# Kernel tuning notes

Measured on AMD Instinct MI355X. Metric: run time of the kernel, lower is better.

Reference implementation:

```python
import jax, jax.numpy as jnp
import numpy as np

N, E = 10000, 160000          # nodes, support edges
CIN, COUT = 32, 32            # channels
R, B = 6, 1                   # radial rings, band limit
M = 2 * B + 1                 # angular frequencies (-B..B)
EPS = 1e-8
PI = float(np.pi)


def _cplx(a):
    # (..., 2) real -> complex64
    return jax.lax.complex(a[..., 0], a[..., 1])


def _reim(z):
    # complex -> (..., 2) real
    return jnp.stack([jnp.real(z), jnp.imag(z)], axis=-1)


def _field_conv(xc, edges, stenc, w, off):
    """FieldConv (ftype=1): real radial/angular weights with per-channel phase offsets.
    xc: (N,Cin) complex, stenc: (E,R,M) complex stencil (transport+quadrature pre-multiplied),
    w: (R,M,Cin,Cout) real, off: (Cin,Cout) phase offsets."""
    Wc = w * jax.lax.complex(jnp.cos(off), jnp.sin(off))[None, None]   # (R,M,Cin,Cout) complex
    src, tgt = edges[:, 0], edges[:, 1]
    # edge gather + complex stencil multiply: (E,R,M,Cin)
    contrib = stenc[:, :, :, None] * xc[src][:, None, None, :]
    # scatter-add to target nodes: (N,R,M,Cin)
    agg = jax.ops.segment_sum(contrib, tgt, num_segments=N)
    # dense per-node filter contraction
    return jnp.einsum('nrmc,rmcd->nd', agg, Wc)


def _tangent_nonlin(xc, b):
    # magnitude ReLU with learned bias, direction preserved (complex tangent features)
    mag = jnp.abs(xc)
    return (jax.nn.relu(mag + b) / jnp.maximum(mag, EPS)) * xc


def _forward(x, supp_edges, supp_sten, w1, off1, b1, w2, off2, b2, res_w):
    xc = _cplx(x)                # (N,CIN) complex64
    stenc = _cplx(supp_sten)     # (E,R,M) complex64
    h = _tangent_nonlin(_field_conv(xc, supp_edges, stenc, w1, off1), b1)
    h = _field_conv(h, supp_edges, stenc, w2, off2)
    y = _tangent_nonlin(xc @ _cplx(res_w) + h, b2)   # residual TangentLin + nonlin
    return _reim(y)              # (N,COUT,2) float32


def setup_inputs() -> dict:
    key = jax.random.key(0)
    ks = jax.random.split(key, 10)
    s1 = 1.0 / np.sqrt(R * M * CIN)
    s2 = 1.0 / np.sqrt(R * M * COUT)
    return {
        'x': jax.random.normal(ks[0], (N, CIN, 2), jnp.float32),
        'supp_edges': jax.random.randint(ks[1], (E, 2), 0, N),
        'supp_sten': 0.1 * jax.random.normal(ks[2], (E, R, M, 2), jnp.float32),
        'w1': s1 * jax.random.normal(ks[3], (R, M, CIN, COUT), jnp.float32),
        'off1': jax.random.uniform(ks[4], (CIN, COUT), jnp.float32, -PI, PI),
        'b1': 0.1 * jax.random.normal(ks[5], (COUT,), jnp.float32),
        'w2': s2 * jax.random.normal(ks[6], (R, M, COUT, COUT), jnp.float32),
        'off2': jax.random.uniform(ks[7], (COUT, COUT), jnp.float32, -PI, PI),
        'b2': 0.1 * jax.random.normal(ks[8], (COUT,), jnp.float32),
        'res_w': (1.0 / np.sqrt(CIN)) * jax.random.normal(ks[9], (CIN, COUT, 2), jnp.float32),
    }


def reference(x, supp_edges, supp_sten, w1, off1, b1, w2, off2, b2, res_w):
    return _forward(x, supp_edges, supp_sten, w1, off1, b1, w2, off2, b2, res_w)
```

## Files before the change

### kernel.cpp

```cpp
#include <hip/hip_runtime.h>
#include <hip/hip_bf16.h>

#define NN   10000
#define EE   160000
#define CINC 32
#define COUTC 32
#define RRR  6
#define MMM  3
#define RM   (RRR*MMM)
#define KK   (RM*CINC)
#define KE   608
#define NPB  4
#define CAP  64
#define AROW 624
#define WSZ  19456
#define EPSV 1e-8f

typedef __attribute__((ext_vector_type(8))) short bf16x8;
typedef __attribute__((ext_vector_type(4))) float f32x4;
typedef __attribute__((ext_vector_type(16))) float f32x16;

__device__ inline short f2bf(float f) {
    __hip_bfloat16 b = __float2bfloat16(f);
    union { __hip_bfloat16 b; short s; } u; u.b = b;
    return u.s;
}
__device__ inline float bf2f(unsigned short h) {
    return __uint_as_float(((unsigned)h) << 16);
}
__device__ inline uint2 packsplit(float re, float im) {
    unsigned short rh = (unsigned short)f2bf(re);
    unsigned short rl = (unsigned short)f2bf(re - bf2f(rh));
    unsigned short ih = (unsigned short)f2bf(im);
    unsigned short il = (unsigned short)f2bf(im - bf2f(ih));
    return make_uint2((unsigned)rh | ((unsigned)rl << 16),
                      (unsigned)ih | ((unsigned)il << 16));
}

__global__ void __launch_bounds__(256)
k_build(const int* __restrict__ edges, int* __restrict__ cursor,
        const float* __restrict__ w1, const float* __restrict__ off1,
        const float* __restrict__ w2, const float* __restrict__ off2,
        short* __restrict__ Wcb1, short* __restrict__ Wcb2,
        int2* __restrict__ sei,
        const float2* __restrict__ xc, uint2* __restrict__ xbf,
        const float2* __restrict__ resw)
{
    int i = blockIdx.x*blockDim.x + threadIdx.x;
    if (i < KK*COUTC) {
        int d = i & 31;
        int k = i >> 5;
        int c = k & 31;
        int r_ = k >> 5;
        int q  = (k >> 3) & 3;
        int kk = k & 7;
        int l  = q*16 + (d & 15);
        int n2 = d >> 4;
        int addr = ((r_*2 + n2)*64 + l)*8 + kk;
        float o1 = off1[c*COUTC + d];
        float o2 = off2[c*COUTC + d];
        float s1 = sinf(o1), c1 = cosf(o1);
        float s2 = sinf(o2), c2 = cosf(o2);
        Wcb1[addr]       = f2bf(w1[i]*c1);
        Wcb1[WSZ + addr] = f2bf(w1[i]*s1);
        Wcb2[addr]       = f2bf(w2[i]*c2);
        Wcb2[WSZ + addr] = f2bf(w2[i]*s2);
    }
    if (i < 1024) {
        int n2 = i >> 9;
        int l2 = (i >> 3) & 63;
        int kk = i & 7;
        int c  = ((l2 >> 4) << 3) + kk;
        int d  = (n2 << 4) + (l2 & 15);
        int addr = ((18*2 + n2)*64 + l2)*8 + kk;
        float2 rv = resw[c*COUTC + d];
        Wcb2[addr]       = f2bf(rv.x);
        Wcb2[WSZ + addr] = f2bf(rv.y);
        Wcb1[addr]       = 0;
        Wcb1[WSZ + addr] = 0;
    }
    if (i < EE) {
        int src = edges[2*i];
        int tgt = edges[2*i+1];
        int pos = atomicAdd(&cursor[tgt], 1);
        if (pos < CAP) sei[tgt*CAP + pos] = make_int2(src, i);
    }
    if (i < NN*CINC) {
        float2 v = xc[i];
        xbf[i] = packsplit(v.x, v.y);
    }
}

template<bool FINAL>
__global__ void __launch_bounds__(256, 4)
k_conv(const uint2* __restrict__ xbf,
       const int*  __restrict__ cnts,
       const int2* __restrict__ sei,
       const float4* __restrict__ stenc4,
       const short* __restrict__ Wcb,
       const float* __restrict__ bias,
       const float2* __restrict__ xres,
       float2* __restrict__ out,
       uint2* __restrict__ outbf)
{
    __shared__ __align__(16) short aggS[2*NPB*AROW];
    int t = threadIdx.x;
    int g = t >> 6;
    int l = t & 63;
    int c = l & 31;
    int oct = l >> 5;
    int n = blockIdx.x*NPB + g;

    f32x16 Pre = (f32x16)(0.f), Pim = (f32x16)(0.f);
    {
        int2 v0 = make_int2(0, 0);
        if (l < 32) v0 = sei[n*CAP + l];
        int cnt = cnts[n]; if (cnt > CAP) cnt = CAP;
        if (l >= 32 && l < cnt) v0 = sei[n*CAP + l];
        int srcAll = (l < cnt) ? v0.x : 0;
        int eidAll = (l < cnt) ? v0.y : 0;

        bool rmok = (c < RM);
        int rmo = ((c >> 1) << 4) + ((c & 1) << 3);
        const char* sb = (const char*)stenc4;
        int ntiles = (cnt + 15) >> 4;

        union P { unsigned u[4]; short s[8]; bf16x8 v; };
        float2 sv[8], svn[8];
        uint2  xv[8], xvn[8];

        auto tload = [&](int ck, float2* svp, uint2* xvp) {
            int ebase = ck*16 + oct*8;
            #pragma unroll
            for (int j = 0; j < 8; ++j) {
                int e = ebase + j;
                int eid = __shfl(eidAll, e, 64);
                int s   = __shfl(srcAll, e, 64);
                bool ok = rmok && (e < cnt);
                float2 vv = make_float2(0.f, 0.f);
                if (ok) vv = *(const float2*)(sb + (size_t)eid*144 + rmo);
                svp[j] = vv;
                xvp[j] = xbf[(s << 5) | c];
            }
        };
        auto tcompute = [&](const float2* svp, const uint2* xvp) {
            P Are, Aim, AimN;
            #pragma unroll
            for (int j = 0; j < 8; ++j) {
                Are.s[j] = f2bf(svp[j].x);
                Aim.s[j] = f2bf(svp[j].y);
            }
            #pragma unroll
            for (int k2 = 0; k2 < 4; ++k2) AimN.u[k2] = Aim.u[k2] ^ 0x80008000u;
            P B;
            #pragma unroll
            for (int k2 = 0; k2 < 4; ++k2)
                B.u[k2] = (xvp[2*k2].x & 0xffffu) | (xvp[2*k2+1].x << 16);
            Pre = __builtin_amdgcn_mfma_f32_32x32x16_bf16(Are.v, B.v, Pre, 0, 0, 0);
            Pim = __builtin_amdgcn_mfma_f32_32x32x16_bf16(Aim.v, B.v, Pim, 0, 0, 0);
            #pragma unroll
            for (int k2 = 0; k2 < 4; ++k2)
                B.u[k2] = (xvp[2*k2].x >> 16) | (xvp[2*k2+1].x & 0xffff0000u);
            Pre = __builtin_amdgcn_mfma_f32_32x32x16_bf16(Are.v, B.v, Pre, 0, 0, 0);
            Pim = __builtin_amdgcn_mfma_f32_32x32x16_bf16(Aim.v, B.v, Pim, 0, 0, 0);
            #pragma unroll
            for (int k2 = 0; k2 < 4; ++k2)
                B.u[k2] = (xvp[2*k2].y & 0xffffu) | (xvp[2*k2+1].y << 16);
            Pre = __builtin_amdgcn_mfma_f32_32x32x16_bf16(AimN.v, B.v, Pre, 0, 0, 0);
            Pim = __builtin_amdgcn_mfma_f32_32x32x16_bf16(Are.v, B.v, Pim, 0, 0, 0);
            #pragma unroll
            for (int k2 = 0; k2 < 4; ++k2)
                B.u[k2] = (xvp[2*k2].y >> 16) | (xvp[2*k2+1].y & 0xffff0000u);
            Pre = __builtin_amdgcn_mfma_f32_32x32x16_bf16(AimN.v, B.v, Pre, 0, 0, 0);
            Pim = __builtin_amdgcn_mfma_f32_32x32x16_bf16(Are.v, B.v, Pim, 0, 0, 0);
        };

        if (ntiles > 0) {
            tload(0, sv, xv);
            for (int ck = 0; ck < ntiles; ++ck) {
                bool more = (ck + 1 < ntiles);
                if (more) tload(ck+1, svn, xvn);
                tcompute(sv, xv);
                if (more) {
                    #pragma unroll
                    for (int j = 0; j < 8; ++j) { sv[j] = svn[j]; xv[j] = xvn[j]; }
                }
            }
        }

        short* aR = aggS + g*AROW;
        short* aI = aggS + NPB*AROW + g*AROW;
        #pragma unroll
        for (int reg = 0; reg < 16; ++reg) {
            int rm = (reg & 3) + 8*(reg >> 2) + 4*oct;
            if (rm < RM) {
                aR[rm*32 + c] = f2bf(Pre[reg]);
                aI[rm*32 + c] = f2bf(Pim[reg]);
            }
        }
        if (l < 32) {
            float2 xvv = make_float2(0.f, 0.f);
            if (FINAL) xvv = xres[(size_t)n*CINC + l];
            aR[KK + l] = f2bf(xvv.x);
            aI[KK + l] = f2bf(xvv.y);
        }
    }
    __syncthreads();

    int quad = l >> 4;
    int nn16 = l & 15;
    int mrow = (nn16 < NPB) ? nn16 : NPB-1;
    int rm0 = (g < 3) ? 5*g : 15;
    int nrm = (g < 3) ? 5 : 4;
    const short* aggR = aggS;
    const short* aggI = aggS + NPB*AROW;
    const short* Wr = Wcb;
    const short* Wi = Wcb + WSZ;
    int lbase = l*8;

    f32x4 Dre[2], Dim[2];
    #pragma unroll
    for (int nt = 0; nt < 2; ++nt) { Dre[nt] = (f32x4)(0.f); Dim[nt] = (f32x4)(0.f); }
    union PU { unsigned u[4]; bf16x8 v; };
    for (int r = rm0; r < rm0 + nrm; ++r) {
        int koff = r*32 + quad*8;
        bf16x8 ar = *(const bf16x8*)(aggR + mrow*AROW + koff);
        PU ai, ain;
        ai.v = *(const bf16x8*)(aggI + mrow*AROW + koff);
        #pragma unroll
        for (int k2 = 0; k2 < 4; ++k2) ain.u[k2] = ai.u[k2] ^ 0x80008000u;
        #pragma unroll
        for (int nt = 0; nt < 2; ++nt) {
            int woff = ((r*2 + nt) << 9) + lbase;
            bf16x8 br = *(const bf16x8*)(Wr + woff);
            bf16x8 bi = *(const bf16x8*)(Wi + woff);
            Dre[nt] = __builtin_amdgcn_mfma_f32_16x16x32_bf16(ar,    br, Dre[nt], 0, 0, 0);
            Dre[nt] = __builtin_amdgcn_mfma_f32_16x16x32_bf16(ain.v, bi, Dre[nt], 0, 0, 0);
            Dim[nt] = __builtin_amdgcn_mfma_f32_16x16x32_bf16(ar,    bi, Dim[nt], 0, 0, 0);
            Dim[nt] = __builtin_amdgcn_mfma_f32_16x16x32_bf16(ai.v,  br, Dim[nt], 0, 0, 0);
        }
    }
    __syncthreads();

    float2* dump = (float2*)aggS;
    if (quad == 0) {
        #pragma unroll
        for (int reg = 0; reg < 4; ++reg) {
            int m = reg;
            #pragma unroll
            for (int nt = 0; nt < 2; ++nt) {
                int d = nt*16 + nn16;
                dump[((size_t)g*NPB + m)*COUTC + d] =
                    make_float2(Dre[nt][reg], Dim[nt][reg]);
            }
        }
    }
    __syncthreads();

    if (t < NPB*COUTC) {
        int m = t >> 5, d = t & 31;
        int nn = blockIdx.x*NPB + m;
        float2 hv = make_float2(0.f, 0.f);
        #pragma unroll
        for (int w = 0; w < NPB; ++w) {
            float2 v = dump[((size_t)w*NPB + m)*COUTC + d];
            hv.x += v.x; hv.y += v.y;
        }
        float mag = sqrtf(hv.x*hv.x + hv.y*hv.y);
        float num = mag + bias[d]; if (num < 0.f) num = 0.f;
        float den = (mag > EPSV) ? mag : EPSV;
        float f = num / den;
        if (FINAL) out[(size_t)nn*COUTC + d] = make_float2(f*hv.x, f*hv.y);
        else       outbf[(size_t)nn*COUTC + d] = packsplit(f*hv.x, f*hv.y);
    }
}

extern "C" void kernel_launch(void* const* d_in, const int* in_sizes, int n_in,
                              void* d_out, int out_size, void* d_ws, size_t ws_size,
                              hipStream_t stream) {
    const float2* xc   = (const float2*)d_in[0];
    const int*   edges = (const int*)  d_in[1];
    const float4* stenc4 = (const float4*)d_in[2];
    const float* w1    = (const float*)d_in[3];
    const float* off1  = (const float*)d_in[4];
    const float* b1    = (const float*)d_in[5];
    const float* w2    = (const float*)d_in[6];
    const float* off2  = (const float*)d_in[7];
    const float* b2    = (const float*)d_in[8];
    const float2* resw = (const float2*)d_in[9];
    float2* out = (float2*)d_out;

    char* ws = (char*)d_ws;
    size_t o = 0;
    auto alloc = [&](size_t bytes) {
        o = (o + 255) & ~(size_t)255;
        size_t r = o; o += bytes; return r;
    };
    int*    cursor = (int*)  (ws + alloc(NN*sizeof(int)));
    int2*   sei    = (int2*) (ws + alloc((size_t)NN*CAP*sizeof(int2)));
    short*  Wcb1   = (short*)(ws + alloc((size_t)2*WSZ*sizeof(short)));
    short*  Wcb2   = (short*)(ws + alloc((size_t)2*WSZ*sizeof(short)));
    uint2*  xbf    = (uint2*)(ws + alloc((size_t)NN*CINC*sizeof(uint2)));
    uint2*  hbf    = (uint2*)(ws + alloc((size_t)NN*CINC*sizeof(uint2)));
    (void)ws_size; (void)in_sizes; (void)n_in; (void)out_size;

    hipMemsetAsync(cursor, 0, NN*sizeof(int), stream);
    k_build<<<(NN*CINC + 255)/256, 256, 0, stream>>>(edges, cursor, w1, off1, w2, off2,
                                                     Wcb1, Wcb2, sei, xc, xbf, resw);

    k_conv<false><<<NN/NPB, 256, 0, stream>>>(xbf, cursor, sei, stenc4,
                                              Wcb1, b1, nullptr, nullptr, hbf);
    k_conv<true> <<<NN/NPB, 256, 0, stream>>>(hbf, cursor, sei, stenc4,
                                              Wcb2, b2, xc, out, nullptr);
}
```

Baseline: 139.4 us.

## Fuse build and both conv passes into one cooperative persistent kernel

Replaces the memset, build kernel and two conv launches with a single cooperative kernel that uses grid-wide syncs between phases and persistent blocks looping over node blocks. It is meant to remove launch gaps and per-launch overhead between the four stages. The cost is grid.sync overhead, the grid size being capped by occupancy, and the loss of the FINAL template specialization, since the flag is now a runtime bool. Occupancy is queried once and cached in a static variable.

```diff
diff --git a/kernel.cpp b/kernel.cpp
--- a/kernel.cpp
+++ b/kernel.cpp
@@ -1,5 +1,8 @@
 #include <hip/hip_runtime.h>
 #include <hip/hip_bf16.h>
+#include <hip/hip_cooperative_groups.h>
+
+namespace cg = cooperative_groups;
 
 #define NN   10000
 #define EE   160000
@@ -11,6 +14,7 @@
 #define KK   (RM*CINC)
 #define KE   608
 #define NPB  4
+#define NVB  (NN/NPB)
 #define CAP  64
 #define AROW 624
 #define WSZ  19456
@@ -37,79 +41,25 @@
                       (unsigned)ih | ((unsigned)il << 16));
 }
 
-__global__ void __launch_bounds__(256)
-k_build(const int* __restrict__ edges, int* __restrict__ cursor,
-        const float* __restrict__ w1, const float* __restrict__ off1,
-        const float* __restrict__ w2, const float* __restrict__ off2,
-        short* __restrict__ Wcb1, short* __restrict__ Wcb2,
-        int2* __restrict__ sei,
-        const float2* __restrict__ xc, uint2* __restrict__ xbf,
-        const float2* __restrict__ resw)
+__device__ __forceinline__ void conv_block(
+    bool fin, int vb,
+    const uint2* __restrict__ xin,
+    const int*  __restrict__ cnts,
+    const int2* __restrict__ sei,
+    const float4* __restrict__ stenc4,
+    const short* __restrict__ Wcb,
+    const float* __restrict__ bias,
+    const float2* __restrict__ xres,
+    float2* __restrict__ out,
+    uint2* __restrict__ outbf,
+    short* aggS)
 {
-    int i = blockIdx.x*blockDim.x + threadIdx.x;
-    if (i < KK*COUTC) {
-        int d = i & 31;
-        int k = i >> 5;
-        int c = k & 31;
-        int r_ = k >> 5;
-        int q  = (k >> 3) & 3;
-        int kk = k & 7;
-        int l  = q*16 + (d & 15);
-        int n2 = d >> 4;
-        int addr = ((r_*2 + n2)*64 + l)*8 + kk;
-        float o1 = off1[c*COUTC + d];
-        float o2 = off2[c*COUTC + d];
-        float s1 = sinf(o1), c1 = cosf(o1);
-        float s2 = sinf(o2), c2 = cosf(o2);
-        Wcb1[addr]       = f2bf(w1[i]*c1);
-        Wcb1[WSZ + addr] = f2bf(w1[i]*s1);
-        Wcb2[addr]       = f2bf(w2[i]*c2);
-        Wcb2[WSZ + addr] = f2bf(w2[i]*s2);
-    }
-    if (i < 1024) {
-        int n2 = i >> 9;
-        int l2 = (i >> 3) & 63;
-        int kk = i & 7;
-        int c  = ((l2 >> 4) << 3) + kk;
-        int d  = (n2 << 4) + (l2 & 15);
-        int addr = ((18*2 + n2)*64 + l2)*8 + kk;
-        float2 rv = resw[c*COUTC + d];
-        Wcb2[addr]       = f2bf(rv.x);
-        Wcb2[WSZ + addr] = f2bf(rv.y);
-        Wcb1[addr]       = 0;
-        Wcb1[WSZ + addr] = 0;
-    }
-    if (i < EE) {
-        int src = edges[2*i];
-        int tgt = edges[2*i+1];
-        int pos = atomicAdd(&cursor[tgt], 1);
-        if (pos < CAP) sei[tgt*CAP + pos] = make_int2(src, i);
-    }
-    if (i < NN*CINC) {
-        float2 v = xc[i];
-        xbf[i] = packsplit(v.x, v.y);
-    }
-}
-
-template<bool FINAL>
-__global__ void __launch_bounds__(256, 4)
-k_conv(const uint2* __restrict__ xbf,
-       const int*  __restrict__ cnts,
-       const int2* __restrict__ sei,
-       const float4* __restrict__ stenc4,
-       const short* __restrict__ Wcb,
-       const float* __restrict__ bias,
-       const float2* __restrict__ xres,
-       float2* __restrict__ out,
-       uint2* __restrict__ outbf)
-{
-    __shared__ __align__(16) short aggS[2*NPB*AROW];
     int t = threadIdx.x;
     int g = t >> 6;
     int l = t & 63;
     int c = l & 31;
     int oct = l >> 5;
-    int n = blockIdx.x*NPB + g;
+    int n = vb*NPB + g;
 
     f32x16 Pre = (f32x16)(0.f), Pim = (f32x16)(0.f);
     {
@@ -140,7 +90,7 @@
                 float2 vv = make_float2(0.f, 0.f);
                 if (ok) vv = *(const float2*)(sb + (size_t)eid*144 + rmo);
                 svp[j] = vv;
-                xvp[j] = xbf[(s << 5) | c];
+                xvp[j] = xin[(s << 5) | c];
             }
         };
         auto tcompute = [&](const float2* svp, const uint2* xvp) {
@@ -200,7 +150,7 @@
         }
         if (l < 32) {
             float2 xvv = make_float2(0.f, 0.f);
-            if (FINAL) xvv = xres[(size_t)n*CINC + l];
+            if (fin) xvv = xres[(size_t)n*CINC + l];
             aR[KK + l] = f2bf(xvv.x);
             aI[KK + l] = f2bf(xvv.y);
         }
@@ -259,7 +209,7 @@
 
     if (t < NPB*COUTC) {
         int m = t >> 5, d = t & 31;
-        int nn = blockIdx.x*NPB + m;
+        int nn = vb*NPB + m;
         float2 hv = make_float2(0.f, 0.f);
         #pragma unroll
         for (int w = 0; w < NPB; ++w) {
@@ -270,16 +220,96 @@
         float num = mag + bias[d]; if (num < 0.f) num = 0.f;
         float den = (mag > EPSV) ? mag : EPSV;
         float f = num / den;
-        if (FINAL) out[(size_t)nn*COUTC + d] = make_float2(f*hv.x, f*hv.y);
-        else       outbf[(size_t)nn*COUTC + d] = packsplit(f*hv.x, f*hv.y);
+        if (fin) out[(size_t)nn*COUTC + d] = make_float2(f*hv.x, f*hv.y);
+        else     outbf[(size_t)nn*COUTC + d] = packsplit(f*hv.x, f*hv.y);
+    }
+}
+
+__global__ void __launch_bounds__(256, 4)
+k_mega(const int* __restrict__ edges, int* __restrict__ cursor,
+       const float* __restrict__ w1, const float* __restrict__ off1,
+       const float* __restrict__ w2, const float* __restrict__ off2,
+       short* __restrict__ Wcb1, short* __restrict__ Wcb2,
+       int2* __restrict__ sei,
+       const float2* __restrict__ xc, uint2* __restrict__ xbf,
+       const float2* __restrict__ resw,
+       const float4* __restrict__ stenc4,
+       const float* __restrict__ b1, const float* __restrict__ b2,
+       uint2* __restrict__ hbf, float2* __restrict__ out)
+{
+    cg::grid_group grid = cg::this_grid();
+    __shared__ __align__(16) short aggS[2*NPB*AROW];
+    int gtid = blockIdx.x*blockDim.x + threadIdx.x;
+    int gsz  = gridDim.x*blockDim.x;
+
+    for (int i = gtid; i < NN; i += gsz) cursor[i] = 0;
+    grid.sync();
+
+    for (int i = gtid; i < NN*CINC; i += gsz) {
+        if (i < KK*COUTC) {
+            int d = i & 31;
+            int k = i >> 5;
+            int c = k & 31;
+            int r_ = k >> 5;
+            int q  = (k >> 3) & 3;
+            int kk = k & 7;
+            int l  = q*16 + (d & 15);
+            int n2 = d >> 4;
+            int addr = ((r_*2 + n2)*64 + l)*8 + kk;
+            float o1 = off1[c*COUTC + d];
+            float o2 = off2[c*COUTC + d];
+            float s1 = sinf(o1), c1 = cosf(o1);
+            float s2 = sinf(o2), c2 = cosf(o2);
+            Wcb1[addr]       = f2bf(w1[i]*c1);
+            Wcb1[WSZ + addr] = f2bf(w1[i]*s1);
+            Wcb2[addr]       = f2bf(w2[i]*c2);
+            Wcb2[WSZ + addr] = f2bf(w2[i]*s2);
+        }
+        if (i < 1024) {
+            int n2 = i >> 9;
+            int l2 = (i >> 3) & 63;
+            int kk = i & 7;
+            int c  = ((l2 >> 4) << 3) + kk;
+            int d  = (n2 << 4) + (l2 & 15);
+            int addr = ((18*2 + n2)*64 + l2)*8 + kk;
+            float2 rv = resw[c*COUTC + d];
+            Wcb2[addr]       = f2bf(rv.x);
+            Wcb2[WSZ + addr] = f2bf(rv.y);
+            Wcb1[addr]       = 0;
+            Wcb1[WSZ + addr] = 0;
+        }
+        if (i < EE) {
+            int src = edges[2*i];
+            int tgt = edges[2*i+1];
+            int pos = atomicAdd(&cursor[tgt], 1);
+            if (pos < CAP) sei[tgt*CAP + pos] = make_int2(src, i);
+        }
+        if (i < NN*CINC) {
+            float2 v = xc[i];
+            xbf[i] = packsplit(v.x, v.y);
+        }
+    }
+    grid.sync();
+
+    for (int vb = blockIdx.x; vb < NVB; vb += gridDim.x) {
+        conv_block(false, vb, xbf, cursor, sei, stenc4, Wcb1, b1,
+                   xc, out, hbf, aggS);
+        __syncthreads();
+    }
+    grid.sync();
+
+    for (int vb = blockIdx.x; vb < NVB; vb += gridDim.x) {
+        conv_block(true, vb, hbf, cursor, sei, stenc4, Wcb2, b2,
+                   xc, out, hbf, aggS);
+        __syncthreads();
     }
 }
 
 extern "C" void kernel_launch(void* const* d_in, const int* in_sizes, int n_in,
                               void* d_out, int out_size, void* d_ws, size_t ws_size,
                               hipStream_t stream) {
+    const int*   edges = (const int*)  d_in[1];
     const float2* xc   = (const float2*)d_in[0];
-    const int*   edges = (const int*)  d_in[1];
     const float4* stenc4 = (const float4*)d_in[2];
     const float* w1    = (const float*)d_in[3];
     const float* off1  = (const float*)d_in[4];
@@ -304,12 +334,31 @@
     uint2*  hbf    = (uint2*)(ws + alloc((size_t)NN*CINC*sizeof(uint2)));
     (void)ws_size; (void)in_sizes; (void)n_in; (void)out_size;
 
-    hipMemsetAsync(cursor, 0, NN*sizeof(int), stream);
-    k_build<<<(NN*CINC + 255)/256, 256, 0, stream>>>(edges, cursor, w1, off1, w2, off2,
-                                                     Wcb1, Wcb2, sei, xc, xbf, resw);
-
-    k_conv<false><<<NN/NPB, 256, 0, stream>>>(xbf, cursor, sei, stenc4,
-                                              Wcb1, b1, nullptr, nullptr, hbf);
-    k_conv<true> <<<NN/NPB, 256, 0, stream>>>(hbf, cursor, sei, stenc4,
-                                              Wcb2, b2, xc, out, nullptr);
-}
+    static int nblk = 0;
+    if (nblk == 0) {
+        int maxb = 0;
+        hipOccupancyMaxActiveBlocksPerMultiprocessor(&maxb, k_mega, 256, 0);
+        int ncu = 256;
+        hipDeviceProp_t prop;
+        int dev = 0;
+        if (hipGetDevice(&dev) == hipSuccess &&
+            hipGetDeviceProperties(&prop, dev) == hipSuccess)
+            ncu = prop.multiProcessorCount;
+        if (maxb < 1) maxb = 4;
+        nblk = maxb * ncu;
+        if (nblk > NVB) nblk = NVB;
+        if (nblk < 64) nblk = 64;
+    }
+
+    void* args[] = {
+        (void*)&edges, (void*)&cursor,
+        (void*)&w1, (void*)&off1, (void*)&w2, (void*)&off2,
+        (void*)&Wcb1, (void*)&Wcb2, (void*)&sei,
+        (void*)&xc, (void*)&xbf, (void*)&resw,
+        (void*)&stenc4,
+        (void*)&b1, (void*)&b2,
+        (void*)&hbf, (void*)&out
+    };
+    hipLaunchCooperativeKernel((const void*)k_mega, dim3(nblk), dim3(256),
+                               args, 0, stream);
+}
```

After: 371.1 us. +166.1%, slower.
